# Kernel tuning notes

Measured on AMD Instinct MI355X. Metric: run time of the kernel, lower is better.

Reference implementation:

```python
import jax, jax.numpy as jnp
import numpy as np

B, S = 32, 4096
HID, MEM, ATT = 512, 512, 512


def setup_inputs() -> dict:
    key = jax.random.key(0)
    k1, k2, k3, k4, k5, k6, k7 = jax.random.split(key, 7)
    scale_h = 1.0 / np.sqrt(HID)
    scale_m = 1.0 / np.sqrt(MEM)
    scale_a = 1.0 / np.sqrt(ATT)
    return {
        "hidden": jax.random.normal(k1, (B, HID), dtype=jnp.float32),
        "memory": jax.random.normal(k2, (B, S, MEM), dtype=jnp.float32),
        "mem_pad": jnp.zeros((B, S), dtype=jnp.bool_),
        "coverage": jax.random.uniform(k3, (B, S), dtype=jnp.float32),
        # params stored as (in, out) so x @ W == torch Linear(x)
        "W_h": jax.random.uniform(k4, (HID, ATT), minval=-scale_h, maxval=scale_h, dtype=jnp.float32),
        "W_m": jax.random.uniform(k5, (MEM, ATT), minval=-scale_m, maxval=scale_m, dtype=jnp.float32),
        "W_c": jax.random.uniform(k6, (ATT,), minval=-1.0, maxval=1.0, dtype=jnp.float32),
        "v": jax.random.uniform(k7, (ATT,), minval=-scale_a, maxval=scale_a, dtype=jnp.float32),
    }


def reference(hidden, memory, mem_pad, coverage, W_h, W_m, W_c, v):
    h = hidden @ W_h                                   # (B, A)
    m = jnp.einsum('bsd,da->bsa', memory, W_m)         # (B, S, A)
    c_feat = coverage[..., None] * W_c                 # (B, S, A) ; Linear(1->A) == scalar * weight row
    score = jnp.einsum('bsa,a->bs', jnp.tanh(h[:, None, :] + m + c_feat), v)  # (B, S)
    score = jnp.where(mem_pad, -jnp.inf, score)
    attn_weights = jax.nn.softmax(score, axis=-1)      # (B, S)
    context = jnp.einsum('bs,bsd->bd', attn_weights, memory)  # (B, D)
    return context, attn_weights
```

## Files before the change

kernel.cpp:

```cpp
#include <hip/hip_runtime.h>
#include <hip/hip_bf16.h>
#include <math.h>

#define BB 32
#define SS 4096
#define DMEM 512
#define DATT 512

typedef short short8 __attribute__((ext_vector_type(8)));
typedef short short4v __attribute__((ext_vector_type(4)));
typedef float floatx4 __attribute__((ext_vector_type(4)));

__device__ inline short f2bf(float x) {
    unsigned u = __float_as_uint(x);
    unsigned r = (u + 0x7fffu + ((u >> 16) & 1u)) >> 16;
    return (short)(r & 0xffffu);
}

__device__ inline float fast_tanh(float x) {
    float e = __expf(2.0f * x);
    return 1.0f - 2.0f / (e + 1.0f);
}

__device__ inline short8 cvt8(float4 lo, float4 hi) {
    union { __hip_bfloat162 h2; unsigned u; } a, b, c, d;
    a.h2 = __float22bfloat162_rn(make_float2(lo.x, lo.y));
    b.h2 = __float22bfloat162_rn(make_float2(lo.z, lo.w));
    c.h2 = __float22bfloat162_rn(make_float2(hi.x, hi.y));
    d.h2 = __float22bfloat162_rn(make_float2(hi.z, hi.w));
    union { unsigned u[4]; short8 s; } r;
    r.u[0] = a.u; r.u[1] = b.u; r.u[2] = c.u; r.u[3] = d.u;
    return r.s;
}

__device__ inline void gld_lds16(const void* g, void* l) {
    __builtin_amdgcn_global_load_lds(
        (const __attribute__((address_space(1))) unsigned int*)g,
        (__attribute__((address_space(3))) unsigned int*)l, 16, 0, 0);
}


__global__ void prep_wt_kernel(const float* __restrict__ Wm, short* __restrict__ Wt) {
    const int n0 = blockIdx.x * 32;
    const int k0 = blockIdx.y * 32;
    const int t = threadIdx.x;
    const int r = t >> 5, c = t & 31;
    __shared__ float lds[32 * 33];
#pragma unroll
    for (int j = 0; j < 4; ++j) {
        int kk = r + j * 8;
        lds[kk * 33 + c] = Wm[(size_t)(k0 + kk) * 512 + n0 + c];
    }
    __syncthreads();
#pragma unroll
    for (int j = 0; j < 4; ++j) {
        int nn = r + j * 8;
        Wt[(size_t)(n0 + nn) * 512 + k0 + c] = f2bf(lds[c * 33 + nn]);
    }
}

__global__ void prep_h_kernel(const float* __restrict__ hidden, const float* __restrict__ Wh,
                              float* __restrict__ h) {
    const int b = blockIdx.x;
    const int n = blockIdx.y * 256 + threadIdx.x;
    const int kc = blockIdx.z;
    float acc = 0.f;
#pragma unroll 8
    for (int k = kc * 128; k < kc * 128 + 128; ++k)
        acc += hidden[b * 512 + k] * Wh[(size_t)k * 512 + n];
    atomicAdd(&h[b * 512 + n], acc);
}


__global__ __launch_bounds__(256, 3)
void score_kernel(const float* __restrict__ memory,
                  const float* __restrict__ coverage,
                  const short* __restrict__ Wt,
                  const float* __restrict__ h,
                  const float* __restrict__ Wc,
                  const float* __restrict__ v,
                  float* __restrict__ scoreParts) {
    const int g = blockIdx.x;
    const int inner = g & 7;
    const int nt = (g >> 3) & 3;
    const int stb = (g >> 5) * 8 + inner;
    const int st = stb & 31;
    const int b = stb >> 5;
    const int n0 = nt * 128;
    const int s0 = st * 128;

    const int tid = threadIdx.x;
    const int lane = tid & 63;
    const int wave = tid >> 6;
    const int wm = wave & 1;
    const int wn = wave >> 1;
    const int col = lane & 15;
    const int q = lane >> 4;

    __shared__ __align__(16) float tileA[128 * 64];
    __shared__ __align__(16) short tileB[128 * 64];
    __shared__ float covS[128];
    __shared__ float sred[2][128];

    if (tid < 128) covS[tid] = coverage[(size_t)b * SS + s0 + tid];

    const char* gA = (const char*)(memory + ((size_t)b * SS + s0) * 512);
    const char* gB = (const char*)(Wt + (size_t)n0 * 512);
    char* ldsA = (char*)tileA + wave * 1024;
    char* ldsB = (char*)tileB + wave * 1024;

    floatx4 acc[4][4];
#pragma unroll
    for (int mi = 0; mi < 4; ++mi)
#pragma unroll
        for (int ni = 0; ni < 4; ++ni)
            acc[mi][ni] = (floatx4){0.f, 0.f, 0.f, 0.f};

    for (int kt = 0; kt < 8; ++kt) {
        __syncthreads();
#pragma unroll
        for (int it = 0; it < 8; ++it) {
            int ci = it * 256 + tid;
            int row = ci >> 4;
            int gch = (ci & 15) ^ (row & 15);
            gld_lds16(gA + (size_t)row * 2048 + kt * 256 + gch * 16, ldsA + it * 4096);
        }
#pragma unroll
        for (int it = 0; it < 4; ++it) {
            int ci = it * 256 + tid;
            int row = ci >> 3;
            int gch = (ci & 7) ^ (row & 7);
            gld_lds16(gB + (size_t)row * 1024 + kt * 128 + gch * 16, ldsB + it * 4096);
        }
        __syncthreads();

#pragma unroll
        for (int ks = 0; ks < 2; ++ks) {
            short8 af[4], bf[4];
            const int ca = ks * 8 + q * 2;
            const int cb = (ks * 4 + q);
#pragma unroll
            for (int mi = 0; mi < 4; ++mi) {
                int row = wm * 64 + mi * 16 + col;
                const float4* pA = (const float4*)tileA + row * 16;
                float4 lo = pA[ca ^ (row & 15)];
                float4 hi = pA[(ca + 1) ^ (row & 15)];
                af[mi] = cvt8(lo, hi);
            }
#pragma unroll
            for (int ni = 0; ni < 4; ++ni) {
                int row = wn * 64 + ni * 16 + col;
                bf[ni] = *(const short8*)((const char*)tileB + row * 128 + ((cb ^ (row & 7)) * 16));
            }
#pragma unroll
            for (int mi = 0; mi < 4; ++mi)
#pragma unroll
                for (int ni = 0; ni < 4; ++ni)
                    acc[mi][ni] = __builtin_amdgcn_mfma_f32_16x16x32_bf16(af[mi], bf[ni], acc[mi][ni], 0, 0, 0);
        }
    }

    float hv[4], wcv[4], vv[4];
#pragma unroll
    for (int ni = 0; ni < 4; ++ni) {
        int n = n0 + wn * 64 + ni * 16 + col;
        hv[ni] = h[b * 512 + n];
        wcv[ni] = Wc[n];
        vv[ni] = v[n];
    }
    float rowAcc[4][4];
#pragma unroll
    for (int mi = 0; mi < 4; ++mi)
#pragma unroll
        for (int r = 0; r < 4; ++r)
            rowAcc[mi][r] = 0.f;
#pragma unroll
    for (int mi = 0; mi < 4; ++mi) {
#pragma unroll
        for (int r = 0; r < 4; ++r) {
            float cv = covS[wm * 64 + mi * 16 + q * 4 + r];
#pragma unroll
            for (int ni = 0; ni < 4; ++ni) {
                float val = acc[mi][ni][r] + hv[ni] + cv * wcv[ni];
                rowAcc[mi][r] += fast_tanh(val) * vv[ni];
            }
        }
    }
#pragma unroll
    for (int off = 1; off < 16; off <<= 1)
#pragma unroll
        for (int mi = 0; mi < 4; ++mi)
#pragma unroll
            for (int r = 0; r < 4; ++r)
                rowAcc[mi][r] += __shfl_xor(rowAcc[mi][r], off, 64);

    if (col == 0) {
#pragma unroll
        for (int mi = 0; mi < 4; ++mi)
#pragma unroll
            for (int r = 0; r < 4; ++r)
                sred[wn][wm * 64 + mi * 16 + q * 4 + r] = rowAcc[mi][r];
    }
    __syncthreads();
    if (tid < 128)
        scoreParts[(size_t)nt * BB * SS + (size_t)b * SS + s0 + tid] =
            sred[0][tid] + sred[1][tid];
}

__global__ void softmax_kernel(const float* __restrict__ scoreParts,
                               const unsigned char* __restrict__ pad,
                               float* __restrict__ attn_out) {
    const int b = blockIdx.x;
    const int tid = threadIdx.x;
    const int wave = tid >> 6, lane = tid & 63;
    __shared__ float redMax[16];
    __shared__ float redSum[16];

    float vals[4];
    float mx = -INFINITY;
#pragma unroll
    for (int i = 0; i < 4; ++i) {
        size_t idx = (size_t)b * SS + tid + i * 1024;
        float s = scoreParts[idx] + scoreParts[(size_t)BB * SS + idx]
                + scoreParts[2 * (size_t)BB * SS + idx] + scoreParts[3 * (size_t)BB * SS + idx];
        if (pad[idx]) s = -INFINITY;
        vals[i] = s;
        mx = fmaxf(mx, s);
    }
#pragma unroll
    for (int off = 32; off >= 1; off >>= 1) mx = fmaxf(mx, __shfl_xor(mx, off, 64));
    if (lane == 0) redMax[wave] = mx;
    __syncthreads();
    float gmax = -INFINITY;
#pragma unroll
    for (int w = 0; w < 16; ++w) gmax = fmaxf(gmax, redMax[w]);

    float sum = 0.f;
#pragma unroll
    for (int i = 0; i < 4; ++i) {
        float e = __expf(vals[i] - gmax);
        vals[i] = e;
        sum += e;
    }
#pragma unroll
    for (int off = 32; off >= 1; off >>= 1) sum += __shfl_xor(sum, off, 64);
    if (lane == 0) redSum[wave] = sum;
    __syncthreads();
    float gsum = 0.f;
#pragma unroll
    for (int w = 0; w < 16; ++w) gsum += redSum[w];
    const float inv = 1.0f / gsum;
#pragma unroll
    for (int i = 0; i < 4; ++i)
        attn_out[(size_t)b * SS + tid + i * 1024] = vals[i] * inv;
}

__global__ __launch_bounds__(256)
void context_kernel(const float* __restrict__ memory,
                    const float* __restrict__ attn,
                    float* __restrict__ ctx) {
    const int sc = blockIdx.x;
    const int dh = blockIdx.y;
    const int b  = blockIdx.z;
    const int t = threadIdx.x;
    const int c = t & 63;
    const int r = t >> 6;

    __shared__ float wS[128];
    __shared__ float4 red[3][64];

    if (t < 128) wS[t] = attn[(size_t)b * SS + sc * 128 + t];
    __syncthreads();

    const float4* m4 = (const float4*)(memory + ((size_t)b * SS + sc * 128) * DMEM) + dh * 64 + c;
    float4 acc = {0.f, 0.f, 0.f, 0.f};
#pragma unroll 8
    for (int i = 0; i < 32; ++i) {
        int row = i * 4 + r;
        float w = wS[row];
        float4 f = m4[(size_t)row * 128];
        acc.x += w * f.x; acc.y += w * f.y; acc.z += w * f.z; acc.w += w * f.w;
    }
    if (r > 0) red[r - 1][c] = acc;
    __syncthreads();
    if (r == 0) {
#pragma unroll
        for (int j = 0; j < 3; ++j) {
            float4 o = red[j][c];
            acc.x += o.x; acc.y += o.y; acc.z += o.z; acc.w += o.w;
        }
        float* dst = &ctx[b * 512 + dh * 256 + c * 4];
        atomicAdd(dst + 0, acc.x);
        atomicAdd(dst + 1, acc.y);
        atomicAdd(dst + 2, acc.z);
        atomicAdd(dst + 3, acc.w);
    }
}

extern "C" void kernel_launch(void* const* d_in, const int* in_sizes, int n_in,
                              void* d_out, int out_size, void* d_ws, size_t ws_size,
                              hipStream_t stream) {
    (void)in_sizes; (void)n_in; (void)out_size; (void)ws_size;
    const float* hidden   = (const float*)d_in[0];
    const float* memory   = (const float*)d_in[1];
    const unsigned char* mem_pad = (const unsigned char*)d_in[2];
    const float* coverage = (const float*)d_in[3];
    const float* Wh       = (const float*)d_in[4];
    const float* Wm       = (const float*)d_in[5];
    const float* Wc       = (const float*)d_in[6];
    const float* v        = (const float*)d_in[7];

    char* ws = (char*)d_ws;
    short* Wt    = (short*)ws;
    float* h     = (float*)(ws + 512 * 1024);
    float* parts = (float*)(ws + 576 * 1024);

    float* ctx  = (float*)d_out;
    float* attn = (float*)d_out + BB * 512;

    hipMemsetAsync(ctx, 0, BB * 512 * sizeof(float), stream);
    hipMemsetAsync(h, 0, BB * 512 * sizeof(float), stream);
    prep_wt_kernel<<<dim3(16, 16), dim3(256), 0, stream>>>(Wm, Wt);
    prep_h_kernel<<<dim3(32, 2, 4), dim3(256), 0, stream>>>(hidden, Wh, h);
    score_kernel<<<dim3(4096), dim3(256), 0, stream>>>(memory, coverage, Wt, h, Wc, v, parts);
    softmax_kernel<<<dim3(BB), dim3(1024), 0, stream>>>(parts, mem_pad, attn);
    context_kernel<<<dim3(32, 2, BB), dim3(256), 0, stream>>>(memory, attn, ctx);
}
```

Before: 501.0 us.

## Register-prefetch A tile and double-buffer B in the score GEMM

The A operand (fp32 memory) is now loaded into registers one k-step ahead, converted to bf16 once per element, and stored into a padded bf16 LDS tile. Previously each wave converted fp32 from LDS for every fragment. The B weight tile is double-buffered through direct global-to-LDS loads so the next stage's fetch overlaps the MFMA work. The goal is to hide global load latency and cut LDS traffic and footprint for A. In exchange it uses more registers for the prefetch and adds a second barrier per iteration.

After: 538.5 us. 1.07x slower.

```diff
diff --git a/kernel.cpp b/kernel.cpp
--- a/kernel.cpp
+++ b/kernel.cpp
@@ -8,7 +8,6 @@
 #define DATT 512
 
 typedef short short8 __attribute__((ext_vector_type(8)));
-typedef short short4v __attribute__((ext_vector_type(4)));
 typedef float floatx4 __attribute__((ext_vector_type(4)));
 
 __device__ inline short f2bf(float x) {
@@ -20,17 +19,6 @@
 __device__ inline float fast_tanh(float x) {
     float e = __expf(2.0f * x);
     return 1.0f - 2.0f / (e + 1.0f);
-}
-
-__device__ inline short8 cvt8(float4 lo, float4 hi) {
-    union { __hip_bfloat162 h2; unsigned u; } a, b, c, d;
-    a.h2 = __float22bfloat162_rn(make_float2(lo.x, lo.y));
-    b.h2 = __float22bfloat162_rn(make_float2(lo.z, lo.w));
-    c.h2 = __float22bfloat162_rn(make_float2(hi.x, hi.y));
-    d.h2 = __float22bfloat162_rn(make_float2(hi.z, hi.w));
-    union { unsigned u[4]; short8 s; } r;
-    r.u[0] = a.u; r.u[1] = b.u; r.u[2] = c.u; r.u[3] = d.u;
-    return r.s;
 }
 
 __device__ inline void gld_lds16(const void* g, void* l) {
@@ -97,17 +85,22 @@
     const int col = lane & 15;
     const int q = lane >> 4;
 
-    __shared__ __align__(16) float tileA[128 * 64];
-    __shared__ __align__(16) short tileB[128 * 64];
+    __shared__ __align__(16) short tileA[128 * 72];
+    __shared__ __align__(16) short tileB[2][128 * 64];
     __shared__ float covS[128];
     __shared__ float sred[2][128];
 
     if (tid < 128) covS[tid] = coverage[(size_t)b * SS + s0 + tid];
 
-    const char* gA = (const char*)(memory + ((size_t)b * SS + s0) * 512);
+    const float4* gA4 = (const float4*)(memory + ((size_t)b * SS + s0) * 512);
     const char* gB = (const char*)(Wt + (size_t)n0 * 512);
-    char* ldsA = (char*)tileA + wave * 1024;
-    char* ldsB = (char*)tileB + wave * 1024;
+
+    const int ar0 = tid >> 4;
+    const int ac16 = tid & 15;
+    const int br0 = tid >> 3;
+    const int bc0 = tid & 7;
+
+    float4 apf[8];
 
     floatx4 acc[4][4];
 #pragma unroll
@@ -116,47 +109,84 @@
         for (int ni = 0; ni < 4; ++ni)
             acc[mi][ni] = (floatx4){0.f, 0.f, 0.f, 0.f};
 
+#pragma unroll
+    for (int i = 0; i < 8; ++i) {
+        int row = i * 16 + ar0;
+        apf[i] = gA4[(size_t)row * 128 + ac16];
+    }
+    {
+        char* ldsB = (char*)(&tileB[0][0]) + wave * 1024;
+#pragma unroll
+        for (int it = 0; it < 4; ++it) {
+            int row = it * 32 + br0;
+            int gch = bc0 ^ (row & 7);
+            gld_lds16(gB + (size_t)row * 1024 + gch * 16, ldsB + it * 4096);
+        }
+    }
+#pragma unroll
+    for (int i = 0; i < 8; ++i) {
+        int row = i * 16 + ar0;
+        union { __hip_bfloat162 h2; unsigned u; } p0, p1;
+        p0.h2 = __float22bfloat162_rn(make_float2(apf[i].x, apf[i].y));
+        p1.h2 = __float22bfloat162_rn(make_float2(apf[i].z, apf[i].w));
+        uint2 w; w.x = p0.u; w.y = p1.u;
+        *(uint2*)((char*)tileA + row * 144 + ac16 * 8) = w;
+    }
+    __syncthreads();
+
     for (int kt = 0; kt < 8; ++kt) {
-        __syncthreads();
-#pragma unroll
-        for (int it = 0; it < 8; ++it) {
-            int ci = it * 256 + tid;
-            int row = ci >> 4;
-            int gch = (ci & 15) ^ (row & 15);
-            gld_lds16(gA + (size_t)row * 2048 + kt * 256 + gch * 16, ldsA + it * 4096);
-        }
-#pragma unroll
-        for (int it = 0; it < 4; ++it) {
-            int ci = it * 256 + tid;
-            int row = ci >> 3;
-            int gch = (ci & 7) ^ (row & 7);
-            gld_lds16(gB + (size_t)row * 1024 + kt * 128 + gch * 16, ldsB + it * 4096);
-        }
-        __syncthreads();
-
+        if (kt < 7) {
+#pragma unroll
+            for (int i = 0; i < 8; ++i) {
+                int row = i * 16 + ar0;
+                apf[i] = gA4[(size_t)row * 128 + (kt + 1) * 16 + ac16];
+            }
+            char* ldsB = (char*)(&tileB[(kt + 1) & 1][0]) + wave * 1024;
+#pragma unroll
+            for (int it = 0; it < 4; ++it) {
+                int row = it * 32 + br0;
+                int gch = bc0 ^ (row & 7);
+                gld_lds16(gB + (size_t)row * 1024 + (kt + 1) * 128 + gch * 16,
+                          ldsB + it * 4096);
+            }
+        }
+
+        const char* bbase = (const char*)(&tileB[kt & 1][0]);
 #pragma unroll
         for (int ks = 0; ks < 2; ++ks) {
             short8 af[4], bf[4];
-            const int ca = ks * 8 + q * 2;
-            const int cb = (ks * 4 + q);
+            const int ca = ks * 64 + q * 16;
+            const int cb = ks * 4 + q;
 #pragma unroll
             for (int mi = 0; mi < 4; ++mi) {
                 int row = wm * 64 + mi * 16 + col;
-                const float4* pA = (const float4*)tileA + row * 16;
-                float4 lo = pA[ca ^ (row & 15)];
-                float4 hi = pA[(ca + 1) ^ (row & 15)];
-                af[mi] = cvt8(lo, hi);
+                af[mi] = *(const short8*)((const char*)tileA + row * 144 + ca);
             }
 #pragma unroll
             for (int ni = 0; ni < 4; ++ni) {
                 int row = wn * 64 + ni * 16 + col;
-                bf[ni] = *(const short8*)((const char*)tileB + row * 128 + ((cb ^ (row & 7)) * 16));
+                bf[ni] = *(const short8*)(bbase + row * 128 + ((cb ^ (row & 7)) * 16));
             }
 #pragma unroll
             for (int mi = 0; mi < 4; ++mi)
 #pragma unroll
                 for (int ni = 0; ni < 4; ++ni)
                     acc[mi][ni] = __builtin_amdgcn_mfma_f32_16x16x32_bf16(af[mi], bf[ni], acc[mi][ni], 0, 0, 0);
+        }
+
+        __syncthreads();
+
+        if (kt < 7) {
+#pragma unroll
+            for (int i = 0; i < 8; ++i) {
+                int row = i * 16 + ar0;
+                union { __hip_bfloat162 h2; unsigned u; } p0, p1;
+                p0.h2 = __float22bfloat162_rn(make_float2(apf[i].x, apf[i].y));
+                p1.h2 = __float22bfloat162_rn(make_float2(apf[i].z, apf[i].w));
+                uint2 w; w.x = p0.u; w.y = p1.u;
+                *(uint2*)((char*)tileA + row * 144 + ac16 * 8) = w;
+            }
+            __syncthreads();
         }
     }
 
```
